# Performance work log

Measured on AMD Instinct MI355X. Metric: run time of the kernel, lower is better.

The kernel has to match this reference:

```python
import jax, jax.numpy as jnp
import numpy as np

B, C, H, W, N = 4, 128, 240, 320, 1024
LEVEL = 8.0          # scaling[0] = 4 * img_scale with img_scale=2
E1_LAMDA = 1.0
E2_LAMDA = 2.0 / 7.0
GN_LAMDA = 0.3
EPS = 1e-9


def extract_features(f, coords):
    # f: (B,C,H,W); coords: (B,N,2) float pixel coords as (x, y)
    Bf, Cf, Hf, Wf = f.shape
    x = coords[..., 0]
    y = coords[..., 1]
    x0 = jnp.floor(x)
    y0 = jnp.floor(y)
    wx = (x - x0)[:, None, :]          # (B,1,N)
    wy = (y - y0)[:, None, :]
    x0i = jnp.clip(x0.astype(jnp.int32), 0, Wf - 1)
    x1i = jnp.clip(x0i + 1, 0, Wf - 1)
    y0i = jnp.clip(y0.astype(jnp.int32), 0, Hf - 1)
    y1i = jnp.clip(y0i + 1, 0, Hf - 1)

    def g(fm, yi, xi):                 # fm: (C,H,W), yi/xi: (N,)
        return fm[:, yi, xi]           # (C,N)

    v00 = jax.vmap(g)(f, y0i, x0i)
    v01 = jax.vmap(g)(f, y0i, x1i)
    v10 = jax.vmap(g)(f, y1i, x0i)
    v11 = jax.vmap(g)(f, y1i, x1i)
    out = (v00 * (1 - wx) * (1 - wy) + v01 * wx * (1 - wy)
           + v10 * (1 - wx) * wy + v11 * wx * wy)          # (B,C,N)
    return out.transpose(0, 2, 1).reshape(Bf * coords.shape[1], Cf)


def l2_normalize(f):
    n = jnp.linalg.norm(f, axis=1, keepdims=True)
    return f / jnp.maximum(n, 1e-12)


def torch_gradient(f):
    # central differences with edge replication; gx = d/dx (width), gy = d/dy (height)
    fpx = jnp.pad(f, ((0, 0), (0, 0), (0, 0), (1, 1)), mode='edge')
    fpy = jnp.pad(f, ((0, 0), (0, 0), (1, 1), (0, 0)), mode='edge')
    gx = 0.5 * (fpx[..., 2:] - fpx[..., :-2])
    gy = 0.5 * (fpy[..., 2:, :] - fpy[..., :-2, :])
    return gx, gy


def compute_gn_loss(f_t, fb, ub, noise):
    Bn, Nn, _ = ub.shape
    xs = (2.0 * noise - 1.0) + ub                   # uniform(-1,1) jitter
    f_s = extract_features(fb, xs)
    f_t = l2_normalize(f_t)
    f_s = l2_normalize(f_s)
    r = f_s - f_t                                   # (BN, C)
    gx, gy = torch_gradient(fb)
    Jx = extract_features(gx, xs)                   # (BN, C)
    Jy = extract_features(gy, xs)
    J = jnp.stack([Jx, Jy], axis=-1)                # (BN, C, 2)
    Hm = jnp.einsum('bci,bcj->bij', J, J) + EPS * jnp.eye(2, dtype=J.dtype)
    b = jnp.einsum('bci,bc->bi', J, r)[..., None]   # (BN, 2, 1)
    # closed-form 2x2 inverse
    a = Hm[:, 0, 0]; bb = Hm[:, 0, 1]; c = Hm[:, 1, 0]; d = Hm[:, 1, 1]
    det = a * d - bb * c
    Hinv = jnp.stack([jnp.stack([d, -bb], -1),
                      jnp.stack([-c, a], -1)], -2) / det[:, None, None]
    miu = xs.reshape(Bn * Nn, 2, 1) - Hinv @ b
    diff = (ub.reshape(Bn * Nn, 2, 1) - miu)[..., 0]          # (BN, 2)
    e1 = 0.5 * jnp.sum(jnp.einsum('bi,bij,bj->b', diff, Hm, diff))
    log_det = jnp.log(det)
    e2 = Bn * Nn * jnp.log(jnp.asarray(2.0 * np.pi, dtype=det.dtype)) - 0.5 * jnp.sum(log_det)
    e = E1_LAMDA * e1 + E2_LAMDA * e2
    return e, e1, e2


def setup_inputs() -> dict:
    key = jax.random.key(0)
    k = jax.random.split(key, 7)
    F_a = jax.random.normal(k[0], (B, C, H, W), dtype=jnp.float32)
    F_b = jax.random.normal(k[1], (B, C, H, W), dtype=jnp.float32)
    # full-resolution match coords, safely inside the map after /LEVEL
    xa = jax.random.uniform(k[2], (B, N)) * (W - 5) * LEVEL + 2 * LEVEL
    ya = jax.random.uniform(k[3], (B, N)) * (H - 5) * LEVEL + 2 * LEVEL
    xb = jax.random.uniform(k[4], (B, N)) * (W - 5) * LEVEL + 2 * LEVEL
    yb = jax.random.uniform(k[5], (B, N)) * (H - 5) * LEVEL + 2 * LEVEL
    matches_a = jnp.stack([xa, ya], axis=-1)
    matches_b = jnp.stack([xb, yb], axis=-1)
    noise = jax.random.uniform(k[6], (B, N, 2), dtype=jnp.float32)
    return {"F_a": F_a, "F_b": F_b, "matches_a": matches_a,
            "matches_b": matches_b, "noise": noise}


def reference(F_a, F_b, matches_a, matches_b, noise):
    f_t = extract_features(F_a, matches_a / LEVEL)
    e, e1, e2 = compute_gn_loss(f_t, F_b, matches_b / LEVEL, noise)
    return GN_LAMDA * e, e1, e2
```

## Files before the change

### kernel.cpp

```cpp
#include <hip/hip_runtime.h>
#include <math.h>

#define B_  4
#define C_  128
#define H_  240
#define W_  320
#define N_  1024
#define NPTS (B_ * N_)
#define HW_ (H_ * W_)
#define NBINS 960

typedef float f4 __attribute__((ext_vector_type(4)));
typedef float f2 __attribute__((ext_vector_type(2)));

__device__ __forceinline__ f4 load4(const float* p) {
    f4 v; __builtin_memcpy(&v, p, 16); return v;
}
__device__ __forceinline__ f2 load2(const float* p) {
    f2 v; __builtin_memcpy(&v, p, 8); return v;
}

__device__ __forceinline__ float wave_reduce(float v) {
    #pragma unroll
    for (int off = 32; off > 0; off >>= 1)
        v += __shfl_xor(v, off, 64);
    return v;
}

__global__ __launch_bounds__(1024) void gn_sort_kernel(
    const float* __restrict__ mb, const float* __restrict__ noise,
    int* __restrict__ perm)
{
    __shared__ int hist[NBINS];
    __shared__ int cursor[NBINS];
    for (int i = threadIdx.x; i < NBINS; i += 1024) hist[i] = 0;
    __syncthreads();

    int mykey[4];
    #pragma unroll
    for (int k = 0; k < 4; ++k) {
        const int p = threadIdx.x + (k << 10);
        const float uby = mb[p * 2 + 1] * 0.125f;
        const float ys  = 2.0f * noise[p * 2 + 1] - 1.0f + uby;
        const int y0 = min(max((int)floorf(ys), 1), H_ - 3);
        mykey[k] = (p >> 10) * H_ + y0;
        atomicAdd(&hist[mykey[k]], 1);
    }
    __syncthreads();

    if (threadIdx.x < 64) {
        const int lane = threadIdx.x;
        const int base = lane * 15;
        int loc[15];
        int s = 0;
        #pragma unroll
        for (int i = 0; i < 15; ++i) { loc[i] = s; s += hist[base + i]; }
        int incl = s;
        #pragma unroll
        for (int off = 1; off < 64; off <<= 1) {
            const int v = __shfl_up(incl, off, 64);
            if (lane >= off) incl += v;
        }
        const int excl = incl - s;
        #pragma unroll
        for (int i = 0; i < 15; ++i) cursor[base + i] = excl + loc[i];
    }
    __syncthreads();

    #pragma unroll
    for (int k = 0; k < 4; ++k) {
        const int p = threadIdx.x + (k << 10);
        const int pos = atomicAdd(&cursor[mykey[k]], 1);
        perm[pos] = p;
    }
}

__global__ __launch_bounds__(256) void gn_point_kernel(
    const float* __restrict__ Fa, const float* __restrict__ Fb,
    const float* __restrict__ ma, const float* __restrict__ mb,
    const float* __restrict__ noise, const int* __restrict__ perm,
    float* __restrict__ ws_e1, float* __restrict__ ws_ld)
{
    const int wid  = threadIdx.x >> 6;
    const int lane = threadIdx.x & 63;
    const int slot = (blockIdx.x << 1) | (wid >> 1);
    const int p = perm[slot];
    const int b = p >> 10;
    const int c = ((wid & 1) << 6) | lane;

    const float inv_level = 0.125f;
    const float xa  = ma[p * 2 + 0] * inv_level;
    const float ya  = ma[p * 2 + 1] * inv_level;
    const float ubx = mb[p * 2 + 0] * inv_level;
    const float uby = mb[p * 2 + 1] * inv_level;
    const float xs  = 2.0f * noise[p * 2 + 0] - 1.0f + ubx;
    const float ys  = 2.0f * noise[p * 2 + 1] - 1.0f + uby;

    const float ax0f = floorf(xa), ay0f = floorf(ya);
    const float awx = xa - ax0f, awy = ya - ay0f;
    const int ax0 = min(max((int)ax0f, 0), W_ - 2);
    const int ay0 = min(max((int)ay0f, 0), H_ - 2);

    const float bx0f = floorf(xs), by0f = floorf(ys);
    const float wx = xs - bx0f, wy = ys - by0f;
    const int x0 = min(max((int)bx0f, 1), W_ - 3);
    const int y0 = min(max((int)by0f, 1), H_ - 3);
    const int xm = x0 - 1;

    const int o_y0 = y0 * W_ + xm;
    const int o_y1 = (y0 + 1) * W_ + xm;
    const int o_ym = (y0 - 1) * W_ + x0;
    const int o_yp = (y0 + 2) * W_ + x0;
    const int o_a0 = ay0 * W_ + ax0;
    const int o_a1 = (ay0 + 1) * W_ + ax0;

    const size_t plane = ((size_t)b * C_ + c) * HW_;
    const float* __restrict__ fa = Fa + plane;
    const float* __restrict__ fb = Fb + plane;

    const f4 row0 = load4(fb + o_y0);
    const f4 row1 = load4(fb + o_y1);
    const f2 rm   = load2(fb + o_ym);
    const f2 rp   = load2(fb + o_yp);
    const f2 a0   = load2(fa + o_a0);
    const f2 a1   = load2(fa + o_a1);

    const float aw00 = (1.f - awx) * (1.f - awy);
    const float aw01 = awx * (1.f - awy);
    const float aw10 = (1.f - awx) * awy;
    const float aw11 = awx * awy;
    const float w00 = (1.f - wx) * (1.f - wy);
    const float w01 = wx * (1.f - wy);
    const float w10 = (1.f - wx) * wy;
    const float w11 = wx * wy;

    const float ft = a0.x * aw00 + a0.y * aw01 + a1.x * aw10 + a1.y * aw11;
    const float fs = row0.y * w00 + row0.z * w01 + row1.y * w10 + row1.z * w11;
    const float jx = 0.5f * ((row0.z - row0.x) * w00 + (row0.w - row0.y) * w01
                           + (row1.z - row1.x) * w10 + (row1.w - row1.y) * w11);
    const float jy = 0.5f * ((row1.y - rm.x) * w00 + (row1.z - rm.y) * w01
                           + (rp.x - row0.y) * w10 + (rp.y - row0.z) * w11);

    float vals[9];
    vals[0] = ft * ft;
    vals[1] = fs * fs;
    vals[2] = jx * fs;
    vals[3] = jx * ft;
    vals[4] = jy * fs;
    vals[5] = jy * ft;
    vals[6] = jx * jx;
    vals[7] = jx * jy;
    vals[8] = jy * jy;

    #pragma unroll
    for (int k = 0; k < 9; ++k)
        vals[k] = wave_reduce(vals[k]);

    __shared__ float sm[4][9];
    if (lane == 0) {
        #pragma unroll
        for (int k = 0; k < 9; ++k) sm[wid][k] = vals[k];
    }
    __syncthreads();

    if ((threadIdx.x & 127) == 0) {
        float s[9];
        #pragma unroll
        for (int k = 0; k < 9; ++k) s[k] = sm[wid][k] + sm[wid + 1][k];

        const float nt = fmaxf(sqrtf(s[0]), 1e-12f);
        const float ns = fmaxf(sqrtf(s[1]), 1e-12f);
        const float b0 = s[2] / ns - s[3] / nt;
        const float b1 = s[4] / ns - s[5] / nt;
        const float H00 = s[6] + 1e-9f;
        const float H01 = s[7];
        const float H11 = s[8] + 1e-9f;
        const float det = H00 * H11 - H01 * H01;
        const float inv = 1.0f / det;
        const float u0 = (H11 * b0 - H01 * b1) * inv;
        const float u1 = (H00 * b1 - H01 * b0) * inv;
        const float d0 = (ubx - xs) + u0;
        const float d1 = (uby - ys) + u1;
        const float quad = d0 * (H00 * d0 + H01 * d1) + d1 * (H01 * d0 + H11 * d1);
        ws_e1[p] = 0.5f * quad;
        ws_ld[p] = logf(det);
    }
}

__global__ __launch_bounds__(256) void gn_reduce_kernel(
    const float* __restrict__ ws_e1, const float* __restrict__ ws_ld,
    float* __restrict__ out)
{
    __shared__ double sm1[256];
    __shared__ double sm2[256];
    double a1 = 0.0, a2 = 0.0;
    for (int i = threadIdx.x; i < NPTS; i += 256) {
        a1 += (double)ws_e1[i];
        a2 += (double)ws_ld[i];
    }
    sm1[threadIdx.x] = a1;
    sm2[threadIdx.x] = a2;
    __syncthreads();
    for (int s = 128; s > 0; s >>= 1) {
        if (threadIdx.x < s) {
            sm1[threadIdx.x] += sm1[threadIdx.x + s];
            sm2[threadIdx.x] += sm2[threadIdx.x + s];
        }
        __syncthreads();
    }
    if (threadIdx.x == 0) {
        const double e1 = sm1[0];
        const double sum_ld = sm2[0];
        const double log2pi = (double)logf(6.283185307179586f);
        const double e2 = (double)NPTS * log2pi - 0.5 * sum_ld;
        const double e = 1.0 * e1 + (2.0 / 7.0) * e2;
        out[0] = (float)(0.3 * e);
        out[1] = (float)e1;
        out[2] = (float)e2;
    }
}

extern "C" void kernel_launch(void* const* d_in, const int* in_sizes, int n_in,
                              void* d_out, int out_size, void* d_ws, size_t ws_size,
                              hipStream_t stream) {
    const float* Fa    = (const float*)d_in[0];
    const float* Fb    = (const float*)d_in[1];
    const float* ma    = (const float*)d_in[2];
    const float* mb    = (const float*)d_in[3];
    const float* noise = (const float*)d_in[4];
    float* out = (float*)d_out;

    float* ws_e1 = (float*)d_ws;
    float* ws_ld = ws_e1 + NPTS;
    int*   perm  = (int*)(ws_ld + NPTS);

    gn_sort_kernel<<<1, 1024, 0, stream>>>(mb, noise, perm);
    gn_point_kernel<<<NPTS / 2, 256, 0, stream>>>(Fa, Fb, ma, mb, noise, perm,
                                                  ws_e1, ws_ld);
    gn_reduce_kernel<<<1, 256, 0, stream>>>(ws_e1, ws_ld, out);
}
```

Measured before the change: 76.93 us.

## Split gather into separate Fa/Fb kernels with per-channel lanes and combine pass

Replaces the single point kernel (one wave per 64 channels of a point, with shuffle reductions) with separate gather kernels for Fa and Fb. In these, each wave covers 64 points sorted by row and two channels per lane, and results go to workspace buffers. A third kernel then reduces over channels per point serially. Fa points get their own row-sorted permutation, which should improve locality for the target gathers. The aim is to drop the cross-lane reductions and make the gathers more cache-friendly. The cost is extra kernel launches and a large intermediate written to and read back from global memory: 2 MB of ft plus 6 MB of fs/jx/jy.

```diff
diff --git a/kernel.cpp b/kernel.cpp
--- a/kernel.cpp
+++ b/kernel.cpp
@@ -19,40 +19,34 @@
 __device__ __forceinline__ f2 load2(const float* p) {
     f2 v; __builtin_memcpy(&v, p, 8); return v;
 }
-
-__device__ __forceinline__ float wave_reduce(float v) {
-    #pragma unroll
-    for (int off = 32; off > 0; off >>= 1)
-        v += __shfl_xor(v, off, 64);
-    return v;
+__device__ __forceinline__ void store2(float* p, f2 v) {
+    __builtin_memcpy(p, &v, 8);
 }
 
 __global__ __launch_bounds__(1024) void gn_sort_kernel(
-    const float* __restrict__ mb, const float* __restrict__ noise,
-    int* __restrict__ perm)
+    const float* __restrict__ ma, const float* __restrict__ mb,
+    const float* __restrict__ noise,
+    int* __restrict__ permA, int* __restrict__ permB)
 {
     __shared__ int hist[NBINS];
     __shared__ int cursor[NBINS];
+
     for (int i = threadIdx.x; i < NBINS; i += 1024) hist[i] = 0;
     __syncthreads();
-
-    int mykey[4];
+    int keyB[4];
     #pragma unroll
     for (int k = 0; k < 4; ++k) {
         const int p = threadIdx.x + (k << 10);
-        const float uby = mb[p * 2 + 1] * 0.125f;
-        const float ys  = 2.0f * noise[p * 2 + 1] - 1.0f + uby;
+        const float ys = 2.0f * noise[p * 2 + 1] - 1.0f + mb[p * 2 + 1] * 0.125f;
         const int y0 = min(max((int)floorf(ys), 1), H_ - 3);
-        mykey[k] = (p >> 10) * H_ + y0;
-        atomicAdd(&hist[mykey[k]], 1);
-    }
-    __syncthreads();
-
+        keyB[k] = (p >> 10) * H_ + y0;
+        atomicAdd(&hist[keyB[k]], 1);
+    }
+    __syncthreads();
     if (threadIdx.x < 64) {
         const int lane = threadIdx.x;
         const int base = lane * 15;
-        int loc[15];
-        int s = 0;
+        int loc[15]; int s = 0;
         #pragma unroll
         for (int i = 0; i < 15; ++i) { loc[i] = s; s += hist[base + i]; }
         int incl = s;
@@ -66,125 +60,201 @@
         for (int i = 0; i < 15; ++i) cursor[base + i] = excl + loc[i];
     }
     __syncthreads();
-
     #pragma unroll
     for (int k = 0; k < 4; ++k) {
         const int p = threadIdx.x + (k << 10);
-        const int pos = atomicAdd(&cursor[mykey[k]], 1);
-        perm[pos] = p;
-    }
-}
-
-__global__ __launch_bounds__(256) void gn_point_kernel(
-    const float* __restrict__ Fa, const float* __restrict__ Fb,
-    const float* __restrict__ ma, const float* __restrict__ mb,
-    const float* __restrict__ noise, const int* __restrict__ perm,
-    float* __restrict__ ws_e1, float* __restrict__ ws_ld)
-{
-    const int wid  = threadIdx.x >> 6;
+        permB[atomicAdd(&cursor[keyB[k]], 1)] = p;
+    }
+    __syncthreads();
+
+    for (int i = threadIdx.x; i < NBINS; i += 1024) hist[i] = 0;
+    __syncthreads();
+    int keyA[4];
+    #pragma unroll
+    for (int k = 0; k < 4; ++k) {
+        const int p = threadIdx.x + (k << 10);
+        const float ya = ma[p * 2 + 1] * 0.125f;
+        const int y0 = min(max((int)floorf(ya), 0), H_ - 2);
+        keyA[k] = (p >> 10) * H_ + y0;
+        atomicAdd(&hist[keyA[k]], 1);
+    }
+    __syncthreads();
+    if (threadIdx.x < 64) {
+        const int lane = threadIdx.x;
+        const int base = lane * 15;
+        int loc[15]; int s = 0;
+        #pragma unroll
+        for (int i = 0; i < 15; ++i) { loc[i] = s; s += hist[base + i]; }
+        int incl = s;
+        #pragma unroll
+        for (int off = 1; off < 64; off <<= 1) {
+            const int v = __shfl_up(incl, off, 64);
+            if (lane >= off) incl += v;
+        }
+        const int excl = incl - s;
+        #pragma unroll
+        for (int i = 0; i < 15; ++i) cursor[base + i] = excl + loc[i];
+    }
+    __syncthreads();
+    #pragma unroll
+    for (int k = 0; k < 4; ++k) {
+        const int p = threadIdx.x + (k << 10);
+        permA[atomicAdd(&cursor[keyA[k]], 1)] = p;
+    }
+}
+
+__global__ __launch_bounds__(256) void gn_ft_kernel(
+    const float* __restrict__ Fa, const float* __restrict__ ma,
+    const int* __restrict__ permA, float* __restrict__ ws_ft)
+{
+    const int w    = (blockIdx.x << 2) | (threadIdx.x >> 6);
     const int lane = threadIdx.x & 63;
-    const int slot = (blockIdx.x << 1) | (wid >> 1);
-    const int p = perm[slot];
-    const int b = p >> 10;
-    const int c = ((wid & 1) << 6) | lane;
-
-    const float inv_level = 0.125f;
-    const float xa  = ma[p * 2 + 0] * inv_level;
-    const float ya  = ma[p * 2 + 1] * inv_level;
-    const float ubx = mb[p * 2 + 0] * inv_level;
-    const float uby = mb[p * 2 + 1] * inv_level;
-    const float xs  = 2.0f * noise[p * 2 + 0] - 1.0f + ubx;
-    const float ys  = 2.0f * noise[p * 2 + 1] - 1.0f + uby;
-
+    const int pg   = w >> 6;
+    const int c0   = (w & 63) << 1;
+    const int p    = permA[(pg << 6) | lane];
+    const int b    = p >> 10;
+
+    const float xa = ma[p * 2 + 0] * 0.125f;
+    const float ya = ma[p * 2 + 1] * 0.125f;
     const float ax0f = floorf(xa), ay0f = floorf(ya);
     const float awx = xa - ax0f, awy = ya - ay0f;
     const int ax0 = min(max((int)ax0f, 0), W_ - 2);
     const int ay0 = min(max((int)ay0f, 0), H_ - 2);
+    const int o0 = ay0 * W_ + ax0;
+    const int o1 = o0 + W_;
+
+    const float* __restrict__ fa0 = Fa + ((size_t)(b * C_ + c0)) * HW_;
+    const float* __restrict__ fa1 = fa0 + HW_;
+
+    const f2 a0_0 = load2(fa0 + o0);
+    const f2 a1_0 = load2(fa0 + o1);
+    const f2 a0_1 = load2(fa1 + o0);
+    const f2 a1_1 = load2(fa1 + o1);
+
+    const float w00 = (1.f - awx) * (1.f - awy);
+    const float w01 = awx * (1.f - awy);
+    const float w10 = (1.f - awx) * awy;
+    const float w11 = awx * awy;
+
+    f2 ft;
+    ft.x = a0_0.x * w00 + a0_0.y * w01 + a1_0.x * w10 + a1_0.y * w11;
+    ft.y = a0_1.x * w00 + a0_1.y * w01 + a1_1.x * w10 + a1_1.y * w11;
+    store2(ws_ft + (size_t)p * C_ + c0, ft);
+}
+
+__global__ __launch_bounds__(256) void gn_fb_kernel(
+    const float* __restrict__ Fb, const float* __restrict__ mb,
+    const float* __restrict__ noise, const int* __restrict__ permB,
+    float* __restrict__ fjp)
+{
+    const int w    = (blockIdx.x << 2) | (threadIdx.x >> 6);
+    const int lane = threadIdx.x & 63;
+    const int pg   = w >> 6;
+    const int c0   = (w & 63) << 1;
+    const int p    = permB[(pg << 6) | lane];
+    const int b    = p >> 10;
+
+    const float ubx = mb[p * 2 + 0] * 0.125f;
+    const float uby = mb[p * 2 + 1] * 0.125f;
+    const float xs  = 2.0f * noise[p * 2 + 0] - 1.0f + ubx;
+    const float ys  = 2.0f * noise[p * 2 + 1] - 1.0f + uby;
 
     const float bx0f = floorf(xs), by0f = floorf(ys);
     const float wx = xs - bx0f, wy = ys - by0f;
     const int x0 = min(max((int)bx0f, 1), W_ - 3);
     const int y0 = min(max((int)by0f, 1), H_ - 3);
-    const int xm = x0 - 1;
-
-    const int o_y0 = y0 * W_ + xm;
-    const int o_y1 = (y0 + 1) * W_ + xm;
+
+    const int o_y0 = y0 * W_ + (x0 - 1);
+    const int o_y1 = o_y0 + W_;
     const int o_ym = (y0 - 1) * W_ + x0;
     const int o_yp = (y0 + 2) * W_ + x0;
-    const int o_a0 = ay0 * W_ + ax0;
-    const int o_a1 = (ay0 + 1) * W_ + ax0;
-
-    const size_t plane = ((size_t)b * C_ + c) * HW_;
-    const float* __restrict__ fa = Fa + plane;
-    const float* __restrict__ fb = Fb + plane;
-
-    const f4 row0 = load4(fb + o_y0);
-    const f4 row1 = load4(fb + o_y1);
-    const f2 rm   = load2(fb + o_ym);
-    const f2 rp   = load2(fb + o_yp);
-    const f2 a0   = load2(fa + o_a0);
-    const f2 a1   = load2(fa + o_a1);
-
-    const float aw00 = (1.f - awx) * (1.f - awy);
-    const float aw01 = awx * (1.f - awy);
-    const float aw10 = (1.f - awx) * awy;
-    const float aw11 = awx * awy;
+
+    const float* __restrict__ fb0 = Fb + ((size_t)(b * C_ + c0)) * HW_;
+    const float* __restrict__ fb1 = fb0 + HW_;
+
+    const f4 r0_0 = load4(fb0 + o_y0);
+    const f4 r1_0 = load4(fb0 + o_y1);
+    const f2 rm_0 = load2(fb0 + o_ym);
+    const f2 rp_0 = load2(fb0 + o_yp);
+    const f4 r0_1 = load4(fb1 + o_y0);
+    const f4 r1_1 = load4(fb1 + o_y1);
+    const f2 rm_1 = load2(fb1 + o_ym);
+    const f2 rp_1 = load2(fb1 + o_yp);
+
     const float w00 = (1.f - wx) * (1.f - wy);
     const float w01 = wx * (1.f - wy);
     const float w10 = (1.f - wx) * wy;
     const float w11 = wx * wy;
 
-    const float ft = a0.x * aw00 + a0.y * aw01 + a1.x * aw10 + a1.y * aw11;
-    const float fs = row0.y * w00 + row0.z * w01 + row1.y * w10 + row1.z * w11;
-    const float jx = 0.5f * ((row0.z - row0.x) * w00 + (row0.w - row0.y) * w01
-                           + (row1.z - row1.x) * w10 + (row1.w - row1.y) * w11);
-    const float jy = 0.5f * ((row1.y - rm.x) * w00 + (row1.z - rm.y) * w01
-                           + (rp.x - row0.y) * w10 + (rp.y - row0.z) * w11);
-
-    float vals[9];
-    vals[0] = ft * ft;
-    vals[1] = fs * fs;
-    vals[2] = jx * fs;
-    vals[3] = jx * ft;
-    vals[4] = jy * fs;
-    vals[5] = jy * ft;
-    vals[6] = jx * jx;
-    vals[7] = jx * jy;
-    vals[8] = jy * jy;
-
-    #pragma unroll
-    for (int k = 0; k < 9; ++k)
-        vals[k] = wave_reduce(vals[k]);
-
-    __shared__ float sm[4][9];
-    if (lane == 0) {
-        #pragma unroll
-        for (int k = 0; k < 9; ++k) sm[wid][k] = vals[k];
-    }
-    __syncthreads();
-
-    if ((threadIdx.x & 127) == 0) {
-        float s[9];
-        #pragma unroll
-        for (int k = 0; k < 9; ++k) s[k] = sm[wid][k] + sm[wid + 1][k];
-
-        const float nt = fmaxf(sqrtf(s[0]), 1e-12f);
-        const float ns = fmaxf(sqrtf(s[1]), 1e-12f);
-        const float b0 = s[2] / ns - s[3] / nt;
-        const float b1 = s[4] / ns - s[5] / nt;
-        const float H00 = s[6] + 1e-9f;
-        const float H01 = s[7];
-        const float H11 = s[8] + 1e-9f;
-        const float det = H00 * H11 - H01 * H01;
-        const float inv = 1.0f / det;
-        const float u0 = (H11 * b0 - H01 * b1) * inv;
-        const float u1 = (H00 * b1 - H01 * b0) * inv;
-        const float d0 = (ubx - xs) + u0;
-        const float d1 = (uby - ys) + u1;
-        const float quad = d0 * (H00 * d0 + H01 * d1) + d1 * (H01 * d0 + H11 * d1);
-        ws_e1[p] = 0.5f * quad;
-        ws_ld[p] = logf(det);
-    }
+    #pragma unroll
+    for (int ch = 0; ch < 2; ++ch) {
+        const f4 row0 = ch ? r0_1 : r0_0;
+        const f4 row1 = ch ? r1_1 : r1_0;
+        const f2 rm   = ch ? rm_1 : rm_0;
+        const f2 rp   = ch ? rp_1 : rp_0;
+        const float fs = row0.y * w00 + row0.z * w01 + row1.y * w10 + row1.z * w11;
+        const float jx = 0.5f * ((row0.z - row0.x) * w00 + (row0.w - row0.y) * w01
+                               + (row1.z - row1.x) * w10 + (row1.w - row1.y) * w11);
+        const float jy = 0.5f * ((row1.y - rm.x) * w00 + (row1.z - rm.y) * w01
+                               + (rp.x - row0.y) * w10 + (rp.y - row0.z) * w11);
+        const size_t base = (size_t)(c0 + ch) * 3 * NPTS + p;
+        fjp[base]            = fs;
+        fjp[base + NPTS]     = jx;
+        fjp[base + 2 * NPTS] = jy;
+    }
+}
+
+__global__ __launch_bounds__(256) void gn_combine_kernel(
+    const float* __restrict__ ws_ft, const float* __restrict__ fjp,
+    const float* __restrict__ mb, const float* __restrict__ noise,
+    float* __restrict__ ws_e1, float* __restrict__ ws_ld)
+{
+    const int p = blockIdx.x * 256 + threadIdx.x;
+
+    float s[9];
+    #pragma unroll
+    for (int k = 0; k < 9; ++k) s[k] = 0.f;
+
+    const float* ftp = ws_ft + (size_t)p * C_;
+    #pragma unroll 4
+    for (int c = 0; c < C_; ++c) {
+        const float ft = ftp[c];
+        const size_t base = (size_t)c * 3 * NPTS + p;
+        const float fs = fjp[base];
+        const float jx = fjp[base + NPTS];
+        const float jy = fjp[base + 2 * NPTS];
+        s[0] += ft * ft;
+        s[1] += fs * fs;
+        s[2] += jx * fs;
+        s[3] += jx * ft;
+        s[4] += jy * fs;
+        s[5] += jy * ft;
+        s[6] += jx * jx;
+        s[7] += jx * jy;
+        s[8] += jy * jy;
+    }
+
+    const float ubx = mb[p * 2 + 0] * 0.125f;
+    const float uby = mb[p * 2 + 1] * 0.125f;
+    const float xs  = 2.0f * noise[p * 2 + 0] - 1.0f + ubx;
+    const float ys  = 2.0f * noise[p * 2 + 1] - 1.0f + uby;
+
+    const float nt = fmaxf(sqrtf(s[0]), 1e-12f);
+    const float ns = fmaxf(sqrtf(s[1]), 1e-12f);
+    const float b0 = s[2] / ns - s[3] / nt;
+    const float b1 = s[4] / ns - s[5] / nt;
+    const float H00 = s[6] + 1e-9f;
+    const float H01 = s[7];
+    const float H11 = s[8] + 1e-9f;
+    const float det = H00 * H11 - H01 * H01;
+    const float inv = 1.0f / det;
+    const float u0 = (H11 * b0 - H01 * b1) * inv;
+    const float u1 = (H00 * b1 - H01 * b0) * inv;
+    const float d0 = (ubx - xs) + u0;
+    const float d1 = (uby - ys) + u1;
+    const float quad = d0 * (H00 * d0 + H01 * d1) + d1 * (H01 * d0 + H11 * d1);
+    ws_e1[p] = 0.5f * quad;
+    ws_ld[p] = logf(det);
 }
 
 __global__ __launch_bounds__(256) void gn_reduce_kernel(
@@ -232,10 +302,15 @@
 
     float* ws_e1 = (float*)d_ws;
     float* ws_ld = ws_e1 + NPTS;
-    int*   perm  = (int*)(ws_ld + NPTS);
-
-    gn_sort_kernel<<<1, 1024, 0, stream>>>(mb, noise, perm);
-    gn_point_kernel<<<NPTS / 2, 256, 0, stream>>>(Fa, Fb, ma, mb, noise, perm,
-                                                  ws_e1, ws_ld);
+    int*   permA = (int*)(ws_ld + NPTS);
+    int*   permB = permA + NPTS;
+    float* ws_ft = (float*)(permB + NPTS);
+    float* fjp   = ws_ft + (size_t)NPTS * C_;
+
+    gn_sort_kernel<<<1, 1024, 0, stream>>>(ma, mb, noise, permA, permB);
+    gn_ft_kernel<<<1024, 256, 0, stream>>>(Fa, ma, permA, ws_ft);
+    gn_fb_kernel<<<1024, 256, 0, stream>>>(Fb, mb, noise, permB, fjp);
+    gn_combine_kernel<<<NPTS / 256, 256, 0, stream>>>(ws_ft, fjp, mb, noise,
+                                                      ws_e1, ws_ld);
     gn_reduce_kernel<<<1, 256, 0, stream>>>(ws_e1, ws_ld, out);
 }
```

Result: faster. 74.52 us (-3.1%).
